# Performance work log

Hardware: AMD Instinct MI355X
Metric: run time of the kernel (lower is better)

Reference implementation:

```python
import jax, jax.numpy as jnp
import numpy as np

N_NODES = 50000
N_GRAPHS = 128
IN_DIM = 512
HID = 512
N_LAYERS = 3


def setup_inputs() -> dict:
    key = jax.random.key(0)
    ks = jax.random.split(key, 12)
    inp = {
        "x": jax.random.normal(ks[0], (N_NODES, IN_DIM), dtype=jnp.float32),
        "walk2": jax.random.randint(ks[1], (3, N_NODES), 0, N_NODES, dtype=jnp.int32),
        "walk3": jax.random.randint(ks[2], (4, N_NODES), 0, N_NODES, dtype=jnp.int32),
        "walk4": jax.random.randint(ks[3], (5, N_NODES), 0, N_NODES, dtype=jnp.int32),
        "batch": jnp.sort(jax.random.randint(ks[4], (N_NODES,), 0, N_GRAPHS, dtype=jnp.int32)),
    }
    dims = [IN_DIM, HID, HID]
    for i in range(N_LAYERS):
        scale = 1.0 / np.sqrt(dims[i])
        inp[f"W{i}"] = jax.random.normal(ks[5 + i], (dims[i], HID), dtype=jnp.float32) * scale
        inp[f"b{i}"] = jnp.zeros((HID,), dtype=jnp.float32)
    return inp


def _gather_sum(z, walk):
    # walk: [L, N] node indices -> sum of gathered embeddings, [N, H]
    L, N = walk.shape
    return jnp.take(z, walk.reshape(-1), axis=0).reshape(L, N, z.shape[1]).sum(0)


def reference(x, walk2, walk3, walk4, batch, W0, b0, W1, b1, W2, b2):
    layers = [(W0, b0), (W1, b1), (W2, b2)]
    path_batch = jnp.take(batch, walk2[0])  # [N]
    counts = jax.ops.segment_sum(jnp.ones((path_batch.shape[0],), jnp.float32),
                                 path_batch, num_segments=N_GRAPHS)
    denom = jnp.maximum(counts, 1.0)[:, None]  # avoid div-by-zero for empty graphs
    z = x
    g = []
    for W, b in layers:
        z = z @ W + b  # [N, H]
        path_emb = _gather_sum(z, walk2) + _gather_sum(z, walk3) + _gather_sum(z, walk4)
        pooled = jax.ops.segment_sum(path_emb, path_batch, num_segments=N_GRAPHS) / denom
        g.append(pooled)
    return jnp.concatenate(g, axis=1)  # [N_GRAPHS, 3*H]
```

## Files before the change

kernel.cpp:

```cpp
#include <hip/hip_runtime.h>

#define N_NODES 50000
#define N_GRAPHS 128
#define HID 512

#define KSPAN   288
#define NSTEP   18
#define KS2     44
#define KSPLIT  (KS2 * 4)
#define KPAD    (KSPAN * KSPLIT)
#define NPANEL  (KPAD / 16)

#define C8_OFF     0
#define C8_BYTES   ((size_t)N_GRAPHS * KPAD)
#define PSUM_OFF   (C8_OFF + C8_BYTES)
#define PSUM_BYTES ((size_t)N_GRAPHS * HID * 4)
#define COUNTS_OFF (PSUM_OFF + PSUM_BYTES)
#define ZERO_BYTES (COUNTS_OFF + 512)
#define APACK_OFF  ZERO_BYTES
#define APACK_BYTES ((size_t)NPANEL * 4 * 64 * 16)
#define PART_OFF   (APACK_OFF + APACK_BYTES)
#define PART_BYTES ((size_t)KS2 * N_GRAPHS * HID * 4)

typedef __attribute__((ext_vector_type(8))) short bf16x8;
typedef __attribute__((ext_vector_type(16))) float f32x16;

__global__ __launch_bounds__(256)
void build_c_kernel(const int* __restrict__ w2, const int* __restrict__ w3,
                    const int* __restrict__ w4, const int* __restrict__ batch,
                    unsigned int* __restrict__ C32, int* __restrict__ counts) {
    __shared__ int hist[N_GRAPHS];
    const int t = threadIdx.x;
    if (t < N_GRAPHS) hist[t] = 0;
    __syncthreads();
    const int i = blockIdx.x * 256 + t;
    if (i < N_NODES) {
        const int a = w2[i];
        const int g = batch[a];
        atomicAdd(&hist[g], 1);
        unsigned int* row = C32 + (size_t)g * (KPAD / 4);
        int nn[12];
        nn[0]  = a;
        nn[1]  = w2[N_NODES + i];
        nn[2]  = w2[2 * N_NODES + i];
        nn[3]  = w3[i];
        nn[4]  = w3[N_NODES + i];
        nn[5]  = w3[2 * N_NODES + i];
        nn[6]  = w3[3 * N_NODES + i];
        nn[7]  = w4[i];
        nn[8]  = w4[N_NODES + i];
        nn[9]  = w4[2 * N_NODES + i];
        nn[10] = w4[3 * N_NODES + i];
        nn[11] = w4[4 * N_NODES + i];
#pragma unroll
        for (int j = 0; j < 12; ++j) {
            const int nd = nn[j];
            atomicAdd(&row[nd >> 2], 1u << ((nd & 3) * 8));
        }
    }
    __syncthreads();
    if (t < N_GRAPHS) { const int hv = hist[t]; if (hv) atomicAdd(&counts[t], hv); }
}

__device__ inline unsigned pack_bf16(unsigned a, unsigned b) {
    return (__builtin_bit_cast(unsigned, (float)a) >> 16) |
           (__builtin_bit_cast(unsigned, (float)b) & 0xFFFF0000u);
}

__global__ __launch_bounds__(256)
void c8_to_apack_kernel(const unsigned char* __restrict__ C8,
                        uint4* __restrict__ Apack) {
    const int kp = blockIdx.x;
    const int t = threadIdx.x;
    const int mt = t >> 6;
    const int l = t & 63;
    const int row = mt * 32 + (l & 31);
    const int k0 = kp * 16 + 8 * (l >> 5);
    const uint2 b = *(const uint2*)(C8 + (size_t)row * KPAD + k0);
    uint4 o;
    o.x = pack_bf16(b.x & 0xFFu, (b.x >> 8) & 0xFFu);
    o.y = pack_bf16((b.x >> 16) & 0xFFu, b.x >> 24);
    o.z = pack_bf16(b.y & 0xFFu, (b.y >> 8) & 0xFFu);
    o.w = pack_bf16((b.y >> 16) & 0xFFu, b.y >> 24);
    Apack[(size_t)(kp * 4 + mt) * 64 + l] = o;
}

template <int GUARD>
__device__ inline void issue_b(const float* __restrict__ xp, int krow,
                               unsigned (&u)[16]) {
#pragma unroll
    for (int j = 0; j < 8; ++j) {
        int k = krow + j;
        if (GUARD) k = min(k, N_NODES - 1);
        const float* p = xp + (size_t)k * HID;
        u[j]     = __builtin_bit_cast(unsigned, p[0]);
        u[8 + j] = __builtin_bit_cast(unsigned, p[32]);
    }
}

__device__ inline f32x16 mfma_bf16(bf16x8 a, bf16x8 b, f32x16 c) {
    return __builtin_amdgcn_mfma_f32_32x32x16_bf16(a, b, c, 0, 0, 0);
}

__device__ inline unsigned bpack(unsigned u0, unsigned u1) {
    return __builtin_amdgcn_perm(u1, u0, 0x07060302u);
}

__device__ inline void step_mfma(const unsigned (&u)[16], const uint4 (&a)[2],
                                 f32x16 (&acc)[2][2]) {
    unsigned d0[4], d1[4];
#pragma unroll
    for (int jj = 0; jj < 4; ++jj) {
        d0[jj] = bpack(u[2 * jj], u[2 * jj + 1]);
        d1[jj] = bpack(u[8 + 2 * jj], u[8 + 2 * jj + 1]);
    }
    const bf16x8 b0 = __builtin_bit_cast(bf16x8, make_uint4(d0[0], d0[1], d0[2], d0[3]));
    const bf16x8 b1 = __builtin_bit_cast(bf16x8, make_uint4(d1[0], d1[1], d1[2], d1[3]));
    const bf16x8 a0 = __builtin_bit_cast(bf16x8, a[0]);
    const bf16x8 a1 = __builtin_bit_cast(bf16x8, a[1]);
    acc[0][0] = mfma_bf16(a0, b0, acc[0][0]);
    acc[0][1] = mfma_bf16(a0, b1, acc[0][1]);
    acc[1][0] = mfma_bf16(a1, b0, acc[1][0]);
    acc[1][1] = mfma_bf16(a1, b1, acc[1][1]);
}

template <int GUARD>
__device__ inline void run_k(const float* __restrict__ xp,
                             const uint4* __restrict__ Apack,
                             int kbase, int h, int lane, int rm,
                             f32x16 (&acc)[2][2]) {
    unsigned bu[3][16];
    uint4 au[3][2];
    const int kp0 = kbase >> 4;
#pragma unroll
    for (int s = 0; s < 3; ++s) {
        issue_b<GUARD>(xp, kbase + s * 16 + 8 * h, bu[s]);
        au[s][0] = Apack[(size_t)((kp0 + s) * 4 + rm * 2) * 64 + lane];
        au[s][1] = Apack[(size_t)((kp0 + s) * 4 + rm * 2 + 1) * 64 + lane];
    }
#pragma unroll
    for (int s = 0; s < NSTEP; ++s) {
        const int slot = s % 3;
        step_mfma(bu[slot], au[slot], acc);
        if (s + 3 < NSTEP) {
            issue_b<GUARD>(xp, kbase + (s + 3) * 16 + 8 * h, bu[slot]);
            au[slot][0] = Apack[(size_t)((kp0 + s + 3) * 4 + rm * 2) * 64 + lane];
            au[slot][1] = Apack[(size_t)((kp0 + s + 3) * 4 + rm * 2 + 1) * 64 + lane];
        }
    }
}

template <int ATOMIC>
__global__ __launch_bounds__(256, 3)
void pool_gemm5_kernel(const float* __restrict__ x,
                       const uint4* __restrict__ Apack,
                       float* __restrict__ dst) {
    __shared__ float red[3][2][64 * 16];
    const int t = threadIdx.x;
    const int lane = t & 63;
    const int w = t >> 6;
    const int n = lane & 31;
    const int h = lane >> 5;
    const int region = blockIdx.x;
    const int rm = region & 1;
    const int rn = region >> 1;
    const int ks = blockIdx.y * 4 + w;
    const int kbase = ks * KSPAN;

    f32x16 acc[2][2];
#pragma unroll
    for (int p = 0; p < 2; ++p)
#pragma unroll
        for (int q = 0; q < 2; ++q)
#pragma unroll
            for (int r = 0; r < 16; ++r) acc[p][q][r] = 0.f;

    const float* xp = x + rn * 64 + n;

    if (kbase + KSPAN <= N_NODES) {
        run_k<0>(xp, Apack, kbase, h, lane, rm, acc);
    } else if (kbase < N_NODES) {
        run_k<1>(xp, Apack, kbase, h, lane, rm, acc);
    }

    float* outp = ATOMIC ? dst : dst + (size_t)blockIdx.y * (N_GRAPHS * HID);
#pragma unroll
    for (int p = 0; p < 2; ++p) {
        __syncthreads();
        if (w > 0) {
#pragma unroll
            for (int q = 0; q < 2; ++q)
#pragma unroll
                for (int i = 0; i < 16; ++i)
                    red[w - 1][q][i * 64 + lane] = acc[p][q][i];
        }
        __syncthreads();
        if (w == 0) {
#pragma unroll
            for (int q = 0; q < 2; ++q)
#pragma unroll
                for (int i = 0; i < 16; ++i) {
                    const float v = acc[p][q][i] + red[0][q][i * 64 + lane] +
                                    red[1][q][i * 64 + lane] + red[2][q][i * 64 + lane];
                    const int row = rm * 64 + p * 32 + (i & 3) + 8 * (i >> 2) + 4 * h;
                    const int col = rn * 64 + q * 32 + n;
                    if (ATOMIC) atomicAdd(&outp[(size_t)row * HID + col], v);
                    else        outp[(size_t)row * HID + col] = v;
                }
        }
    }
}

__global__ __launch_bounds__(256)
void reduce_part_kernel(const float* __restrict__ part, float* __restrict__ Psum) {
    const int id = blockIdx.x * 256 + threadIdx.x;
    float s0 = 0.f, s1 = 0.f;
    for (int k = 0; k + 2 <= KS2; k += 2) {
        s0 += part[(size_t)k * (N_GRAPHS * HID) + id];
        s1 += part[(size_t)(k + 1) * (N_GRAPHS * HID) + id];
    }
    Psum[id] = s0 + s1;
}

__global__ __launch_bounds__(256)
void layer_gemm_kernel(const float* __restrict__ A, int lda, int scaleA,
                       const float* __restrict__ W,
                       const float* __restrict__ bias,
                       const int* __restrict__ counts,
                       float* __restrict__ out) {
    __shared__ float Alds[16][128];
    const int ct = blockIdx.x, rt = blockIdx.y, ksb = blockIdx.z;
    const int t = threadIdx.x;
    const int cc = ct * 64 + (t & 63);
    const int wv = t >> 6;
    const int k0 = ksb * 128;

    for (int idx = t; idx < 16 * 32; idx += 256) {
        const int rr = idx >> 5;
        const int kk = (idx & 31) * 4;
        const int row = rt * 16 + rr;
        float4 v = *(const float4*)&A[(size_t)row * lda + k0 + kk];
        if (scaleA) {
            const float inv = 1.f / (float)max(counts[row], 1);
            v.x *= inv; v.y *= inv; v.z *= inv; v.w *= inv;
        }
        *(float4*)&Alds[rr][kk] = v;
    }
    __syncthreads();

    const int r0 = rt * 16 + wv * 4;
    float a0 = 0.f, a1 = 0.f, a2 = 0.f, a3 = 0.f;
#pragma unroll 8
    for (int k = 0; k < 128; ++k) {
        const float wval = W[(size_t)(k0 + k) * HID + cc];
        a0 += Alds[wv * 4 + 0][k] * wval;
        a1 += Alds[wv * 4 + 1][k] * wval;
        a2 += Alds[wv * 4 + 2][k] * wval;
        a3 += Alds[wv * 4 + 3][k] * wval;
    }
    if (ksb == 0) {
        const float bc = bias[cc];
        a0 += (counts[r0 + 0] > 0 ? 12.f : 0.f) * bc;
        a1 += (counts[r0 + 1] > 0 ? 12.f : 0.f) * bc;
        a2 += (counts[r0 + 2] > 0 ? 12.f : 0.f) * bc;
        a3 += (counts[r0 + 3] > 0 ? 12.f : 0.f) * bc;
    }
    atomicAdd(&out[(size_t)(r0 + 0) * 1536 + cc], a0);
    atomicAdd(&out[(size_t)(r0 + 1) * 1536 + cc], a1);
    atomicAdd(&out[(size_t)(r0 + 2) * 1536 + cc], a2);
    atomicAdd(&out[(size_t)(r0 + 3) * 1536 + cc], a3);
}

extern "C" void kernel_launch(void* const* d_in, const int* in_sizes, int n_in,
                              void* d_out, int out_size, void* d_ws, size_t ws_size,
                              hipStream_t stream) {
    const float* x     = (const float*)d_in[0];
    const int*   w2    = (const int*)d_in[1];
    const int*   w3    = (const int*)d_in[2];
    const int*   w4    = (const int*)d_in[3];
    const int*   batch = (const int*)d_in[4];
    const float* W0    = (const float*)d_in[5];
    const float* b0    = (const float*)d_in[6];
    const float* W1    = (const float*)d_in[7];
    const float* b1    = (const float*)d_in[8];
    const float* W2    = (const float*)d_in[9];
    const float* b2    = (const float*)d_in[10];
    float* out = (float*)d_out;

    unsigned char* ws  = (unsigned char*)d_ws;
    unsigned int* C32  = (unsigned int*)(ws + C8_OFF);
    float* Psum        = (float*)(ws + PSUM_OFF);
    int* counts        = (int*)(ws + COUNTS_OFF);
    uint4* Apack       = (uint4*)(ws + APACK_OFF);
    float* part        = (float*)(ws + PART_OFF);
    const bool use_part = ws_size >= PART_OFF + PART_BYTES;

    hipMemsetAsync(d_ws, 0, ZERO_BYTES, stream);
    hipMemsetAsync(d_out, 0, (size_t)out_size * 4, stream);

    build_c_kernel<<<(N_NODES + 255) / 256, 256, 0, stream>>>(w2, w3, w4, batch, C32, counts);
    c8_to_apack_kernel<<<NPANEL, 256, 0, stream>>>((const unsigned char*)C32, Apack);

    if (use_part) {
        pool_gemm5_kernel<0><<<dim3(16, KS2), 256, 0, stream>>>(x, Apack, part);
        reduce_part_kernel<<<256, 256, 0, stream>>>(part, Psum);
    } else {
        pool_gemm5_kernel<1><<<dim3(16, KS2), 256, 0, stream>>>(x, Apack, Psum);
    }

    layer_gemm_kernel<<<dim3(8, 8, 4), 256, 0, stream>>>(Psum, HID, 1, W0, b0, counts, out);
    layer_gemm_kernel<<<dim3(8, 8, 4), 256, 0, stream>>>(out, 1536, 0, W1, b1, counts, out + 512);
    layer_gemm_kernel<<<dim3(8, 8, 4), 256, 0, stream>>>(out + 512, 1536, 0, W2, b2, counts, out + 1024);
}
```

Measured before the change: 266.4 us.

## Precompose layer weight chain and fuse three layer GEMMs; remap pool blocks per XCD

Because pooling is linear and commutes with the layers, the per-layer weights are precomposed (W0, W0·W1, W0·W1·W2, with bias rows scaled by the path count) into augmented matrices. All three graph outputs then come from one fused GEMM on the pooled input, replacing three dependent layer GEMMs and the output memset. The change also retiles the K split (272 span, 48 groups) and remaps pool GEMM blocks so each XCD handles a contiguous K range. The weight-chain GEMMs are input-independent but recomputed every call, adding work and reassociating float sums, which may shift rounding.

```diff
diff --git a/kernel.cpp b/kernel.cpp
--- a/kernel.cpp
+++ b/kernel.cpp
@@ -4,9 +4,9 @@
 #define N_GRAPHS 128
 #define HID 512
 
-#define KSPAN   288
-#define NSTEP   18
-#define KS2     44
+#define KSPAN   272
+#define NSTEP   17
+#define KS2     48
 #define KSPLIT  (KS2 * 4)
 #define KPAD    (KSPAN * KSPLIT)
 #define NPANEL  (KPAD / 16)
@@ -21,6 +21,8 @@
 #define APACK_BYTES ((size_t)NPANEL * 4 * 64 * 16)
 #define PART_OFF   (APACK_OFF + APACK_BYTES)
 #define PART_BYTES ((size_t)KS2 * N_GRAPHS * HID * 4)
+#define WAUG_OFF   (PART_OFF + PART_BYTES)
+#define WAUG_BYTES ((size_t)3 * 513 * HID * 4)
 
 typedef __attribute__((ext_vector_type(8))) short bf16x8;
 typedef __attribute__((ext_vector_type(16))) float f32x16;
@@ -161,10 +163,15 @@
     const int w = t >> 6;
     const int n = lane & 31;
     const int h = lane >> 5;
-    const int region = blockIdx.x;
+
+    const int lb = blockIdx.x + 16 * blockIdx.y;
+    const int xcd = lb & 7;
+    const int j = lb >> 3;
+    const int region = j & 15;
+    const int ksg = xcd * (KS2 / 8) + (j >> 4);
     const int rm = region & 1;
     const int rn = region >> 1;
-    const int ks = blockIdx.y * 4 + w;
+    const int ks = ksg * 4 + w;
     const int kbase = ks * KSPAN;
 
     f32x16 acc[2][2];
@@ -183,7 +190,7 @@
         run_k<1>(xp, Apack, kbase, h, lane, rm, acc);
     }
 
-    float* outp = ATOMIC ? dst : dst + (size_t)blockIdx.y * (N_GRAPHS * HID);
+    float* outp = ATOMIC ? dst : dst + (size_t)ksg * (N_GRAPHS * HID);
 #pragma unroll
     for (int p = 0; p < 2; ++p) {
         __syncthreads();
@@ -220,6 +227,94 @@
         s1 += part[(size_t)(k + 1) * (N_GRAPHS * HID) + id];
     }
     Psum[id] = s0 + s1;
+}
+
+__global__ __launch_bounds__(256)
+void waug_init_kernel(const float* __restrict__ W0, const float* __restrict__ b0,
+                      float* __restrict__ Aout) {
+    const int id = blockIdx.x * 256 + threadIdx.x;
+    if (id < 512 * 512)      Aout[id] = W0[id];
+    else if (id < 513 * 512) Aout[id] = 12.f * b0[id - 512 * 512];
+}
+
+__global__ __launch_bounds__(256)
+void wchain_kernel(const float* __restrict__ Ain, const float* __restrict__ W,
+                   const float* __restrict__ b, float* __restrict__ Aout) {
+    __shared__ float Alds[16][512];
+    const int t = threadIdx.x;
+    const int ct = blockIdx.x;
+    const int rt = blockIdx.y;
+    const int cc = ct * 64 + (t & 63);
+    for (int idx = t; idx < 16 * 128; idx += 256) {
+        const int rr = idx >> 7;
+        const int kk = (idx & 127) * 4;
+        const int row = rt * 16 + rr;
+        float4 v = (row < 513) ? *(const float4*)&Ain[(size_t)row * 512 + kk]
+                               : make_float4(0.f, 0.f, 0.f, 0.f);
+        *(float4*)&Alds[rr][kk] = v;
+    }
+    __syncthreads();
+    const int wv = t >> 6;
+    float a0 = 0.f, a1 = 0.f, a2 = 0.f, a3 = 0.f;
+#pragma unroll 8
+    for (int k = 0; k < 512; ++k) {
+        const float wval = W[(size_t)k * 512 + cc];
+        a0 += Alds[wv * 4 + 0][k] * wval;
+        a1 += Alds[wv * 4 + 1][k] * wval;
+        a2 += Alds[wv * 4 + 2][k] * wval;
+        a3 += Alds[wv * 4 + 3][k] * wval;
+    }
+    const int r0 = rt * 16 + wv * 4;
+    float acc[4] = {a0, a1, a2, a3};
+#pragma unroll
+    for (int i = 0; i < 4; ++i) {
+        const int row = r0 + i;
+        if (row < 513)
+            Aout[(size_t)row * 512 + cc] = acc[i] + (row == 512 ? 12.f * b[cc] : 0.f);
+    }
+}
+
+__global__ __launch_bounds__(256)
+void fused_layers_kernel(const float* __restrict__ Psum,
+                         const float* __restrict__ Waug,
+                         const int* __restrict__ counts,
+                         float* __restrict__ out) {
+    __shared__ float Alds[16][512];
+    const int t = threadIdx.x;
+    const int ct = blockIdx.x;
+    const int rt = blockIdx.y;
+    const int l = ct >> 3;
+    const int ccl = (ct & 7) * 64 + (t & 63);
+    for (int idx = t; idx < 16 * 128; idx += 256) {
+        const int rr = idx >> 7;
+        const int kk = (idx & 127) * 4;
+        const int row = rt * 16 + rr;
+        float4 v = *(const float4*)&Psum[(size_t)row * 512 + kk];
+        const float inv = 1.f / (float)max(counts[row], 1);
+        v.x *= inv; v.y *= inv; v.z *= inv; v.w *= inv;
+        *(float4*)&Alds[rr][kk] = v;
+    }
+    __syncthreads();
+    const float* W = Waug + (size_t)l * (513 * 512);
+    const int wv = t >> 6;
+    float a0 = 0.f, a1 = 0.f, a2 = 0.f, a3 = 0.f;
+#pragma unroll 8
+    for (int k = 0; k < 512; ++k) {
+        const float wval = W[(size_t)k * 512 + ccl];
+        a0 += Alds[wv * 4 + 0][k] * wval;
+        a1 += Alds[wv * 4 + 1][k] * wval;
+        a2 += Alds[wv * 4 + 2][k] * wval;
+        a3 += Alds[wv * 4 + 3][k] * wval;
+    }
+    const float bv = W[512 * 512 + ccl];
+    const int r0 = rt * 16 + wv * 4;
+    float acc[4] = {a0, a1, a2, a3};
+#pragma unroll
+    for (int i = 0; i < 4; ++i) {
+        const int row = r0 + i;
+        out[(size_t)row * 1536 + l * 512 + ccl] =
+            acc[i] + (counts[row] > 0 ? bv : 0.f);
+    }
 }
 
 __global__ __launch_bounds__(256)
@@ -293,22 +388,38 @@
     int* counts        = (int*)(ws + COUNTS_OFF);
     uint4* Apack       = (uint4*)(ws + APACK_OFF);
     float* part        = (float*)(ws + PART_OFF);
+    float* Waug        = (float*)(ws + WAUG_OFF);
     const bool use_part = ws_size >= PART_OFF + PART_BYTES;
+    const bool use_waug = ws_size >= WAUG_OFF + WAUG_BYTES;
 
     hipMemsetAsync(d_ws, 0, ZERO_BYTES, stream);
-    hipMemsetAsync(d_out, 0, (size_t)out_size * 4, stream);
+    if (!use_waug)
+        hipMemsetAsync(d_out, 0, (size_t)out_size * 4, stream);
 
     build_c_kernel<<<(N_NODES + 255) / 256, 256, 0, stream>>>(w2, w3, w4, batch, C32, counts);
     c8_to_apack_kernel<<<NPANEL, 256, 0, stream>>>((const unsigned char*)C32, Apack);
 
     if (use_part) {
         pool_gemm5_kernel<0><<<dim3(16, KS2), 256, 0, stream>>>(x, Apack, part);
-        reduce_part_kernel<<<256, 256, 0, stream>>>(part, Psum);
     } else {
         pool_gemm5_kernel<1><<<dim3(16, KS2), 256, 0, stream>>>(x, Apack, Psum);
     }
 
-    layer_gemm_kernel<<<dim3(8, 8, 4), 256, 0, stream>>>(Psum, HID, 1, W0, b0, counts, out);
-    layer_gemm_kernel<<<dim3(8, 8, 4), 256, 0, stream>>>(out, 1536, 0, W1, b1, counts, out + 512);
-    layer_gemm_kernel<<<dim3(8, 8, 4), 256, 0, stream>>>(out + 512, 1536, 0, W2, b2, counts, out + 1024);
-}
+    if (use_waug) {
+        waug_init_kernel<<<(513 * 512 + 255) / 256, 256, 0, stream>>>(W0, b0, Waug);
+        wchain_kernel<<<dim3(8, 33), 256, 0, stream>>>(Waug, W1, b1, Waug + 513 * 512);
+        wchain_kernel<<<dim3(8, 33), 256, 0, stream>>>(Waug + 513 * 512, W2, b2,
+                                                       Waug + 2 * 513 * 512);
+    }
+
+    if (use_part)
+        reduce_part_kernel<<<256, 256, 0, stream>>>(part, Psum);
+
+    if (use_waug) {
+        fused_layers_kernel<<<dim3(24, 8), 256, 0, stream>>>(Psum, Waug, counts, out);
+    } else {
+        layer_gemm_kernel<<<dim3(8, 8, 4), 256, 0, stream>>>(Psum, HID, 1, W0, b0, counts, out);
+        layer_gemm_kernel<<<dim3(8, 8, 4), 256, 0, stream>>>(out, 1536, 0, W1, b1, counts, out + 512);
+        layer_gemm_kernel<<<dim3(8, 8, 4), 256, 0, stream>>>(out + 512, 1536, 0, W2, b2, counts, out + 1024);
+    }
+}
```

Result: slower. 333.9 us (+25.3%).

## Fuse count-matrix bf16 packing into pool GEMM and drop layer split-K atomics

Applied to the files above, without the earlier changes.

Removes the separate c8_to_apack kernel. The pool GEMM now reads the uint8 count matrix directly and converts it to bf16 in registers. Each block now covers all 128 graph rows and 32 output columns, so x is read once per column strip instead of twice, at the cost of more redundant A loads and conversions per wave. The layer GEMMs lose their K-split and atomics, write their results directly, and no longer need the output memset; the trade-off is fewer blocks and a longer serial K loop.

```diff
diff --git a/kernel.cpp b/kernel.cpp
--- a/kernel.cpp
+++ b/kernel.cpp
@@ -9,18 +9,16 @@
 #define KS2     44
 #define KSPLIT  (KS2 * 4)
 #define KPAD    (KSPAN * KSPLIT)
-#define NPANEL  (KPAD / 16)
 
 #define C8_OFF     0
 #define C8_BYTES   ((size_t)N_GRAPHS * KPAD)
-#define PSUM_OFF   (C8_OFF + C8_BYTES)
+#define COUNTS_OFF C8_BYTES
+#define PSUM_OFF   (COUNTS_OFF + 512)
 #define PSUM_BYTES ((size_t)N_GRAPHS * HID * 4)
-#define COUNTS_OFF (PSUM_OFF + PSUM_BYTES)
-#define ZERO_BYTES (COUNTS_OFF + 512)
-#define APACK_OFF  ZERO_BYTES
-#define APACK_BYTES ((size_t)NPANEL * 4 * 64 * 16)
-#define PART_OFF   (APACK_OFF + APACK_BYTES)
+#define PART_OFF   (PSUM_OFF + PSUM_BYTES)
 #define PART_BYTES ((size_t)KS2 * N_GRAPHS * HID * 4)
+#define ZERO_MAIN  (COUNTS_OFF + 512)
+#define ZERO_FB    (PSUM_OFF + PSUM_BYTES)
 
 typedef __attribute__((ext_vector_type(8))) short bf16x8;
 typedef __attribute__((ext_vector_type(16))) float f32x16;
@@ -67,146 +65,123 @@
            (__builtin_bit_cast(unsigned, (float)b) & 0xFFFF0000u);
 }
 
-__global__ __launch_bounds__(256)
-void c8_to_apack_kernel(const unsigned char* __restrict__ C8,
-                        uint4* __restrict__ Apack) {
-    const int kp = blockIdx.x;
-    const int t = threadIdx.x;
-    const int mt = t >> 6;
-    const int l = t & 63;
-    const int row = mt * 32 + (l & 31);
-    const int k0 = kp * 16 + 8 * (l >> 5);
-    const uint2 b = *(const uint2*)(C8 + (size_t)row * KPAD + k0);
+template <int GUARD>
+__device__ inline void issue_b(const float* __restrict__ xp, int krow,
+                               unsigned (&u)[8]) {
+#pragma unroll
+    for (int j = 0; j < 8; ++j) {
+        int k = krow + j;
+        if (GUARD) k = min(k, N_NODES - 1);
+        u[j] = __builtin_bit_cast(unsigned, xp[(size_t)k * HID]);
+    }
+}
+
+__device__ inline f32x16 mfma_bf16(bf16x8 a, bf16x8 b, f32x16 c) {
+    return __builtin_amdgcn_mfma_f32_32x32x16_bf16(a, b, c, 0, 0, 0);
+}
+
+__device__ inline unsigned bpack(unsigned u0, unsigned u1) {
+    return __builtin_amdgcn_perm(u1, u0, 0x07060302u);
+}
+
+__device__ inline bf16x8 apack8(uint2 b) {
     uint4 o;
     o.x = pack_bf16(b.x & 0xFFu, (b.x >> 8) & 0xFFu);
     o.y = pack_bf16((b.x >> 16) & 0xFFu, b.x >> 24);
     o.z = pack_bf16(b.y & 0xFFu, (b.y >> 8) & 0xFFu);
     o.w = pack_bf16((b.y >> 16) & 0xFFu, b.y >> 24);
-    Apack[(size_t)(kp * 4 + mt) * 64 + l] = o;
-}
-
-template <int GUARD>
-__device__ inline void issue_b(const float* __restrict__ xp, int krow,
-                               unsigned (&u)[16]) {
-#pragma unroll
-    for (int j = 0; j < 8; ++j) {
-        int k = krow + j;
-        if (GUARD) k = min(k, N_NODES - 1);
-        const float* p = xp + (size_t)k * HID;
-        u[j]     = __builtin_bit_cast(unsigned, p[0]);
-        u[8 + j] = __builtin_bit_cast(unsigned, p[32]);
-    }
-}
-
-__device__ inline f32x16 mfma_bf16(bf16x8 a, bf16x8 b, f32x16 c) {
-    return __builtin_amdgcn_mfma_f32_32x32x16_bf16(a, b, c, 0, 0, 0);
-}
-
-__device__ inline unsigned bpack(unsigned u0, unsigned u1) {
-    return __builtin_amdgcn_perm(u1, u0, 0x07060302u);
-}
-
-__device__ inline void step_mfma(const unsigned (&u)[16], const uint4 (&a)[2],
-                                 f32x16 (&acc)[2][2]) {
-    unsigned d0[4], d1[4];
-#pragma unroll
-    for (int jj = 0; jj < 4; ++jj) {
-        d0[jj] = bpack(u[2 * jj], u[2 * jj + 1]);
-        d1[jj] = bpack(u[8 + 2 * jj], u[8 + 2 * jj + 1]);
-    }
-    const bf16x8 b0 = __builtin_bit_cast(bf16x8, make_uint4(d0[0], d0[1], d0[2], d0[3]));
-    const bf16x8 b1 = __builtin_bit_cast(bf16x8, make_uint4(d1[0], d1[1], d1[2], d1[3]));
-    const bf16x8 a0 = __builtin_bit_cast(bf16x8, a[0]);
-    const bf16x8 a1 = __builtin_bit_cast(bf16x8, a[1]);
-    acc[0][0] = mfma_bf16(a0, b0, acc[0][0]);
-    acc[0][1] = mfma_bf16(a0, b1, acc[0][1]);
-    acc[1][0] = mfma_bf16(a1, b0, acc[1][0]);
-    acc[1][1] = mfma_bf16(a1, b1, acc[1][1]);
+    return __builtin_bit_cast(bf16x8, o);
+}
+
+__device__ inline void step_mfma(const unsigned (&u)[8], const uint2 (&a)[4],
+                                 f32x16 (&acc)[4]) {
+    unsigned d[4];
+#pragma unroll
+    for (int jj = 0; jj < 4; ++jj) d[jj] = bpack(u[2 * jj], u[2 * jj + 1]);
+    const bf16x8 b0 = __builtin_bit_cast(bf16x8, make_uint4(d[0], d[1], d[2], d[3]));
+#pragma unroll
+    for (int mt = 0; mt < 4; ++mt)
+        acc[mt] = mfma_bf16(apack8(a[mt]), b0, acc[mt]);
 }
 
 template <int GUARD>
 __device__ inline void run_k(const float* __restrict__ xp,
-                             const uint4* __restrict__ Apack,
-                             int kbase, int h, int lane, int rm,
-                             f32x16 (&acc)[2][2]) {
-    unsigned bu[3][16];
-    uint4 au[3][2];
-    const int kp0 = kbase >> 4;
+                             const unsigned char* __restrict__ c8p,
+                             int kbase, int h, f32x16 (&acc)[4]) {
+    unsigned bu[3][8];
+    uint2 au[3][4];
 #pragma unroll
     for (int s = 0; s < 3; ++s) {
-        issue_b<GUARD>(xp, kbase + s * 16 + 8 * h, bu[s]);
-        au[s][0] = Apack[(size_t)((kp0 + s) * 4 + rm * 2) * 64 + lane];
-        au[s][1] = Apack[(size_t)((kp0 + s) * 4 + rm * 2 + 1) * 64 + lane];
+        const int kr = kbase + s * 16 + 8 * h;
+        issue_b<GUARD>(xp, kr, bu[s]);
+#pragma unroll
+        for (int mt = 0; mt < 4; ++mt)
+            au[s][mt] = *(const uint2*)(c8p + (size_t)mt * (32 * KPAD) + kr);
     }
 #pragma unroll
     for (int s = 0; s < NSTEP; ++s) {
         const int slot = s % 3;
         step_mfma(bu[slot], au[slot], acc);
         if (s + 3 < NSTEP) {
-            issue_b<GUARD>(xp, kbase + (s + 3) * 16 + 8 * h, bu[slot]);
-            au[slot][0] = Apack[(size_t)((kp0 + s + 3) * 4 + rm * 2) * 64 + lane];
-            au[slot][1] = Apack[(size_t)((kp0 + s + 3) * 4 + rm * 2 + 1) * 64 + lane];
+            const int kr = kbase + (s + 3) * 16 + 8 * h;
+            issue_b<GUARD>(xp, kr, bu[slot]);
+#pragma unroll
+            for (int mt = 0; mt < 4; ++mt)
+                au[slot][mt] = *(const uint2*)(c8p + (size_t)mt * (32 * KPAD) + kr);
         }
     }
 }
 
 template <int ATOMIC>
 __global__ __launch_bounds__(256, 3)
-void pool_gemm5_kernel(const float* __restrict__ x,
-                       const uint4* __restrict__ Apack,
+void pool_gemm6_kernel(const float* __restrict__ x,
+                       const unsigned char* __restrict__ C8,
                        float* __restrict__ dst) {
-    __shared__ float red[3][2][64 * 16];
+    __shared__ float red[3][16 * 64];
     const int t = threadIdx.x;
     const int lane = t & 63;
     const int w = t >> 6;
     const int n = lane & 31;
     const int h = lane >> 5;
-    const int region = blockIdx.x;
-    const int rm = region & 1;
-    const int rn = region >> 1;
+    const int rn = blockIdx.x;
     const int ks = blockIdx.y * 4 + w;
     const int kbase = ks * KSPAN;
 
-    f32x16 acc[2][2];
-#pragma unroll
-    for (int p = 0; p < 2; ++p)
-#pragma unroll
-        for (int q = 0; q < 2; ++q)
-#pragma unroll
-            for (int r = 0; r < 16; ++r) acc[p][q][r] = 0.f;
-
-    const float* xp = x + rn * 64 + n;
+    f32x16 acc[4];
+#pragma unroll
+    for (int p = 0; p < 4; ++p)
+#pragma unroll
+        for (int r = 0; r < 16; ++r) acc[p][r] = 0.f;
+
+    const float* xp = x + rn * 32 + n;
+    const unsigned char* c8p = C8 + (size_t)(lane & 31) * KPAD;
 
     if (kbase + KSPAN <= N_NODES) {
-        run_k<0>(xp, Apack, kbase, h, lane, rm, acc);
+        run_k<0>(xp, c8p, kbase, h, acc);
     } else if (kbase < N_NODES) {
-        run_k<1>(xp, Apack, kbase, h, lane, rm, acc);
+        run_k<1>(xp, c8p, kbase, h, acc);
     }
 
     float* outp = ATOMIC ? dst : dst + (size_t)blockIdx.y * (N_GRAPHS * HID);
 #pragma unroll
-    for (int p = 0; p < 2; ++p) {
+    for (int p = 0; p < 4; ++p) {
         __syncthreads();
         if (w > 0) {
 #pragma unroll
-            for (int q = 0; q < 2; ++q)
-#pragma unroll
-                for (int i = 0; i < 16; ++i)
-                    red[w - 1][q][i * 64 + lane] = acc[p][q][i];
+            for (int i = 0; i < 16; ++i)
+                red[w - 1][i * 64 + lane] = acc[p][i];
         }
         __syncthreads();
         if (w == 0) {
 #pragma unroll
-            for (int q = 0; q < 2; ++q)
-#pragma unroll
-                for (int i = 0; i < 16; ++i) {
-                    const float v = acc[p][q][i] + red[0][q][i * 64 + lane] +
-                                    red[1][q][i * 64 + lane] + red[2][q][i * 64 + lane];
-                    const int row = rm * 64 + p * 32 + (i & 3) + 8 * (i >> 2) + 4 * h;
-                    const int col = rn * 64 + q * 32 + n;
-                    if (ATOMIC) atomicAdd(&outp[(size_t)row * HID + col], v);
-                    else        outp[(size_t)row * HID + col] = v;
-                }
+            for (int i = 0; i < 16; ++i) {
+                const float v = acc[p][i] + red[0][i * 64 + lane] +
+                                red[1][i * 64 + lane] + red[2][i * 64 + lane];
+                const int row = p * 32 + (i & 3) + 8 * (i >> 2) + 4 * h;
+                const int col = rn * 32 + n;
+                if (ATOMIC) atomicAdd(&outp[(size_t)row * HID + col], v);
+                else        outp[(size_t)row * HID + col] = v;
+            }
         }
     }
 }
@@ -223,23 +198,22 @@
 }
 
 __global__ __launch_bounds__(256)
-void layer_gemm_kernel(const float* __restrict__ A, int lda, int scaleA,
-                       const float* __restrict__ W,
-                       const float* __restrict__ bias,
-                       const int* __restrict__ counts,
-                       float* __restrict__ out) {
-    __shared__ float Alds[16][128];
-    const int ct = blockIdx.x, rt = blockIdx.y, ksb = blockIdx.z;
+void layer_gemm6_kernel(const float* __restrict__ A, int lda, int scaleA,
+                        const float* __restrict__ W,
+                        const float* __restrict__ bias,
+                        const int* __restrict__ counts,
+                        float* __restrict__ out) {
+    __shared__ float Alds[16][512];
+    const int ct = blockIdx.x, rt = blockIdx.y;
     const int t = threadIdx.x;
     const int cc = ct * 64 + (t & 63);
     const int wv = t >> 6;
-    const int k0 = ksb * 128;
-
-    for (int idx = t; idx < 16 * 32; idx += 256) {
-        const int rr = idx >> 5;
-        const int kk = (idx & 31) * 4;
+
+    for (int idx = t; idx < 16 * 128; idx += 256) {
+        const int rr = idx >> 7;
+        const int kk = (idx & 127) * 4;
         const int row = rt * 16 + rr;
-        float4 v = *(const float4*)&A[(size_t)row * lda + k0 + kk];
+        float4 v = *(const float4*)&A[(size_t)row * lda + kk];
         if (scaleA) {
             const float inv = 1.f / (float)max(counts[row], 1);
             v.x *= inv; v.y *= inv; v.z *= inv; v.w *= inv;
@@ -251,24 +225,18 @@
     const int r0 = rt * 16 + wv * 4;
     float a0 = 0.f, a1 = 0.f, a2 = 0.f, a3 = 0.f;
 #pragma unroll 8
-    for (int k = 0; k < 128; ++k) {
-        const float wval = W[(size_t)(k0 + k) * HID + cc];
+    for (int k = 0; k < 512; ++k) {
+        const float wval = W[(size_t)k * HID + cc];
         a0 += Alds[wv * 4 + 0][k] * wval;
         a1 += Alds[wv * 4 + 1][k] * wval;
         a2 += Alds[wv * 4 + 2][k] * wval;
         a3 += Alds[wv * 4 + 3][k] * wval;
     }
-    if (ksb == 0) {
-        const float bc = bias[cc];
-        a0 += (counts[r0 + 0] > 0 ? 12.f : 0.f) * bc;
-        a1 += (counts[r0 + 1] > 0 ? 12.f : 0.f) * bc;
-        a2 += (counts[r0 + 2] > 0 ? 12.f : 0.f) * bc;
-        a3 += (counts[r0 + 3] > 0 ? 12.f : 0.f) * bc;
-    }
-    atomicAdd(&out[(size_t)(r0 + 0) * 1536 + cc], a0);
-    atomicAdd(&out[(size_t)(r0 + 1) * 1536 + cc], a1);
-    atomicAdd(&out[(size_t)(r0 + 2) * 1536 + cc], a2);
-    atomicAdd(&out[(size_t)(r0 + 3) * 1536 + cc], a3);
+    const float bc = bias[cc];
+    out[(size_t)(r0 + 0) * 1536 + cc] = a0 + (counts[r0 + 0] > 0 ? 12.f : 0.f) * bc;
+    out[(size_t)(r0 + 1) * 1536 + cc] = a1 + (counts[r0 + 1] > 0 ? 12.f : 0.f) * bc;
+    out[(size_t)(r0 + 2) * 1536 + cc] = a2 + (counts[r0 + 2] > 0 ? 12.f : 0.f) * bc;
+    out[(size_t)(r0 + 3) * 1536 + cc] = a3 + (counts[r0 + 3] > 0 ? 12.f : 0.f) * bc;
 }
 
 extern "C" void kernel_launch(void* const* d_in, const int* in_sizes, int n_in,
@@ -289,26 +257,25 @@
 
     unsigned char* ws  = (unsigned char*)d_ws;
     unsigned int* C32  = (unsigned int*)(ws + C8_OFF);
+    int* counts        = (int*)(ws + COUNTS_OFF);
     float* Psum        = (float*)(ws + PSUM_OFF);
-    int* counts        = (int*)(ws + COUNTS_OFF);
-    uint4* Apack       = (uint4*)(ws + APACK_OFF);
     float* part        = (float*)(ws + PART_OFF);
     const bool use_part = ws_size >= PART_OFF + PART_BYTES;
 
-    hipMemsetAsync(d_ws, 0, ZERO_BYTES, stream);
-    hipMemsetAsync(d_out, 0, (size_t)out_size * 4, stream);
+    hipMemsetAsync(d_ws, 0, use_part ? ZERO_MAIN : ZERO_FB, stream);
 
     build_c_kernel<<<(N_NODES + 255) / 256, 256, 0, stream>>>(w2, w3, w4, batch, C32, counts);
-    c8_to_apack_kernel<<<NPANEL, 256, 0, stream>>>((const unsigned char*)C32, Apack);
 
     if (use_part) {
-        pool_gemm5_kernel<0><<<dim3(16, KS2), 256, 0, stream>>>(x, Apack, part);
+        pool_gemm6_kernel<0><<<dim3(16, KS2), 256, 0, stream>>>(
+            x, (const unsigned char*)C32, part);
         reduce_part_kernel<<<256, 256, 0, stream>>>(part, Psum);
     } else {
-        pool_gemm5_kernel<1><<<dim3(16, KS2), 256, 0, stream>>>(x, Apack, Psum);
-    }
-
-    layer_gemm_kernel<<<dim3(8, 8, 4), 256, 0, stream>>>(Psum, HID, 1, W0, b0, counts, out);
-    layer_gemm_kernel<<<dim3(8, 8, 4), 256, 0, stream>>>(out, 1536, 0, W1, b1, counts, out + 512);
-    layer_gemm_kernel<<<dim3(8, 8, 4), 256, 0, stream>>>(out + 512, 1536, 0, W2, b2, counts, out + 1024);
-}
+        pool_gemm6_kernel<1><<<dim3(16, KS2), 256, 0, stream>>>(
+            x, (const unsigned char*)C32, Psum);
+    }
+
+    layer_gemm6_kernel<<<dim3(8, 8), 256, 0, stream>>>(Psum, HID, 1, W0, b0, counts, out);
+    layer_gemm6_kernel<<<dim3(8, 8), 256, 0, stream>>>(out, 1536, 0, W1, b1, counts, out + 512);
+    layer_gemm6_kernel<<<dim3(8, 8), 256, 0, stream>>>(out + 512, 1536, 0, W2, b2, counts, out + 1024);
+}
```

New measurement: 368.7 us. 1.38x slower.

## Reshape pooling GEMM tiles to cover all 128 graph rows per block

Applied to the files above, without the earlier changes.

Each pooling-GEMM block now computes all 128 graph rows for a 32-column slice, using four MFMA row tiles per wave, instead of a 64x64 tile. Before, every node-feature element of x was fetched by two row regions; now it is fetched once, which halves the dominant x read traffic. The cost is twice as many packed A-operand loads per k-step and a narrower 32-column load per row. The K split is also retuned (span 272, 48 k-groups) to match the new grid.

```diff
diff --git a/kernel.cpp b/kernel.cpp
--- a/kernel.cpp
+++ b/kernel.cpp
@@ -4,9 +4,9 @@
 #define N_GRAPHS 128
 #define HID 512
 
-#define KSPAN   288
-#define NSTEP   18
-#define KS2     44
+#define KSPAN   272
+#define NSTEP   17
+#define KS2     48
 #define KSPLIT  (KS2 * 4)
 #define KPAD    (KSPAN * KSPLIT)
 #define NPANEL  (KPAD / 16)
@@ -86,15 +86,13 @@
 }
 
 template <int GUARD>
-__device__ inline void issue_b(const float* __restrict__ xp, int krow,
-                               unsigned (&u)[16]) {
+__device__ inline void issue_b8(const float* __restrict__ xp, int krow,
+                                unsigned (&u)[8]) {
 #pragma unroll
     for (int j = 0; j < 8; ++j) {
         int k = krow + j;
         if (GUARD) k = min(k, N_NODES - 1);
-        const float* p = xp + (size_t)k * HID;
-        u[j]     = __builtin_bit_cast(unsigned, p[0]);
-        u[8 + j] = __builtin_bit_cast(unsigned, p[32]);
+        u[j] = __builtin_bit_cast(unsigned, xp[(size_t)k * HID]);
     }
 }
 
@@ -106,107 +104,94 @@
     return __builtin_amdgcn_perm(u1, u0, 0x07060302u);
 }
 
-__device__ inline void step_mfma(const unsigned (&u)[16], const uint4 (&a)[2],
-                                 f32x16 (&acc)[2][2]) {
-    unsigned d0[4], d1[4];
-#pragma unroll
-    for (int jj = 0; jj < 4; ++jj) {
-        d0[jj] = bpack(u[2 * jj], u[2 * jj + 1]);
-        d1[jj] = bpack(u[8 + 2 * jj], u[8 + 2 * jj + 1]);
-    }
-    const bf16x8 b0 = __builtin_bit_cast(bf16x8, make_uint4(d0[0], d0[1], d0[2], d0[3]));
-    const bf16x8 b1 = __builtin_bit_cast(bf16x8, make_uint4(d1[0], d1[1], d1[2], d1[3]));
-    const bf16x8 a0 = __builtin_bit_cast(bf16x8, a[0]);
-    const bf16x8 a1 = __builtin_bit_cast(bf16x8, a[1]);
-    acc[0][0] = mfma_bf16(a0, b0, acc[0][0]);
-    acc[0][1] = mfma_bf16(a0, b1, acc[0][1]);
-    acc[1][0] = mfma_bf16(a1, b0, acc[1][0]);
-    acc[1][1] = mfma_bf16(a1, b1, acc[1][1]);
+__device__ inline void step_mfma4(const unsigned (&u)[8], const uint4 (&a)[4],
+                                  f32x16 (&acc)[4]) {
+    unsigned d[4];
+#pragma unroll
+    for (int jj = 0; jj < 4; ++jj) d[jj] = bpack(u[2 * jj], u[2 * jj + 1]);
+    const bf16x8 b0 = __builtin_bit_cast(bf16x8, make_uint4(d[0], d[1], d[2], d[3]));
+#pragma unroll
+    for (int mt = 0; mt < 4; ++mt)
+        acc[mt] = mfma_bf16(__builtin_bit_cast(bf16x8, a[mt]), b0, acc[mt]);
 }
 
 template <int GUARD>
-__device__ inline void run_k(const float* __restrict__ xp,
-                             const uint4* __restrict__ Apack,
-                             int kbase, int h, int lane, int rm,
-                             f32x16 (&acc)[2][2]) {
-    unsigned bu[3][16];
-    uint4 au[3][2];
+__device__ inline void run_k4(const float* __restrict__ xp,
+                              const uint4* __restrict__ Apack,
+                              int kbase, int h, int lane,
+                              f32x16 (&acc)[4]) {
+    unsigned bu[3][8];
+    uint4 au[3][4];
     const int kp0 = kbase >> 4;
 #pragma unroll
     for (int s = 0; s < 3; ++s) {
-        issue_b<GUARD>(xp, kbase + s * 16 + 8 * h, bu[s]);
-        au[s][0] = Apack[(size_t)((kp0 + s) * 4 + rm * 2) * 64 + lane];
-        au[s][1] = Apack[(size_t)((kp0 + s) * 4 + rm * 2 + 1) * 64 + lane];
+        issue_b8<GUARD>(xp, kbase + s * 16 + 8 * h, bu[s]);
+#pragma unroll
+        for (int mt = 0; mt < 4; ++mt)
+            au[s][mt] = Apack[(size_t)((kp0 + s) * 4 + mt) * 64 + lane];
     }
 #pragma unroll
     for (int s = 0; s < NSTEP; ++s) {
         const int slot = s % 3;
-        step_mfma(bu[slot], au[slot], acc);
+        step_mfma4(bu[slot], au[slot], acc);
         if (s + 3 < NSTEP) {
-            issue_b<GUARD>(xp, kbase + (s + 3) * 16 + 8 * h, bu[slot]);
-            au[slot][0] = Apack[(size_t)((kp0 + s + 3) * 4 + rm * 2) * 64 + lane];
-            au[slot][1] = Apack[(size_t)((kp0 + s + 3) * 4 + rm * 2 + 1) * 64 + lane];
+            issue_b8<GUARD>(xp, kbase + (s + 3) * 16 + 8 * h, bu[slot]);
+#pragma unroll
+            for (int mt = 0; mt < 4; ++mt)
+                au[slot][mt] = Apack[(size_t)((kp0 + s + 3) * 4 + mt) * 64 + lane];
         }
     }
 }
 
 template <int ATOMIC>
 __global__ __launch_bounds__(256, 3)
-void pool_gemm5_kernel(const float* __restrict__ x,
+void pool_gemm7_kernel(const float* __restrict__ x,
                        const uint4* __restrict__ Apack,
                        float* __restrict__ dst) {
-    __shared__ float red[3][2][64 * 16];
+    __shared__ float red[3][16 * 64];
     const int t = threadIdx.x;
     const int lane = t & 63;
     const int w = t >> 6;
     const int n = lane & 31;
     const int h = lane >> 5;
-    const int region = blockIdx.x;
-    const int rm = region & 1;
-    const int rn = region >> 1;
+    const int rn = blockIdx.x;
     const int ks = blockIdx.y * 4 + w;
     const int kbase = ks * KSPAN;
 
-    f32x16 acc[2][2];
-#pragma unroll
-    for (int p = 0; p < 2; ++p)
-#pragma unroll
-        for (int q = 0; q < 2; ++q)
-#pragma unroll
-            for (int r = 0; r < 16; ++r) acc[p][q][r] = 0.f;
-
-    const float* xp = x + rn * 64 + n;
+    f32x16 acc[4];
+#pragma unroll
+    for (int p = 0; p < 4; ++p)
+#pragma unroll
+        for (int r = 0; r < 16; ++r) acc[p][r] = 0.f;
+
+    const float* xp = x + rn * 32 + n;
 
     if (kbase + KSPAN <= N_NODES) {
-        run_k<0>(xp, Apack, kbase, h, lane, rm, acc);
+        run_k4<0>(xp, Apack, kbase, h, lane, acc);
     } else if (kbase < N_NODES) {
-        run_k<1>(xp, Apack, kbase, h, lane, rm, acc);
+        run_k4<1>(xp, Apack, kbase, h, lane, acc);
     }
 
     float* outp = ATOMIC ? dst : dst + (size_t)blockIdx.y * (N_GRAPHS * HID);
 #pragma unroll
-    for (int p = 0; p < 2; ++p) {
+    for (int p = 0; p < 4; ++p) {
         __syncthreads();
         if (w > 0) {
 #pragma unroll
-            for (int q = 0; q < 2; ++q)
-#pragma unroll
-                for (int i = 0; i < 16; ++i)
-                    red[w - 1][q][i * 64 + lane] = acc[p][q][i];
+            for (int i = 0; i < 16; ++i)
+                red[w - 1][i * 64 + lane] = acc[p][i];
         }
         __syncthreads();
         if (w == 0) {
 #pragma unroll
-            for (int q = 0; q < 2; ++q)
-#pragma unroll
-                for (int i = 0; i < 16; ++i) {
-                    const float v = acc[p][q][i] + red[0][q][i * 64 + lane] +
-                                    red[1][q][i * 64 + lane] + red[2][q][i * 64 + lane];
-                    const int row = rm * 64 + p * 32 + (i & 3) + 8 * (i >> 2) + 4 * h;
-                    const int col = rn * 64 + q * 32 + n;
-                    if (ATOMIC) atomicAdd(&outp[(size_t)row * HID + col], v);
-                    else        outp[(size_t)row * HID + col] = v;
-                }
+            for (int i = 0; i < 16; ++i) {
+                const float v = acc[p][i] + red[0][i * 64 + lane] +
+                                red[1][i * 64 + lane] + red[2][i * 64 + lane];
+                const int row = p * 32 + (i & 3) + 8 * (i >> 2) + 4 * h;
+                const int col = rn * 32 + n;
+                if (ATOMIC) atomicAdd(&outp[(size_t)row * HID + col], v);
+                else        outp[(size_t)row * HID + col] = v;
+            }
         }
     }
 }
@@ -302,10 +287,10 @@
     c8_to_apack_kernel<<<NPANEL, 256, 0, stream>>>((const unsigned char*)C32, Apack);
 
     if (use_part) {
-        pool_gemm5_kernel<0><<<dim3(16, KS2), 256, 0, stream>>>(x, Apack, part);
+        pool_gemm7_kernel<0><<<dim3(16, KS2), 256, 0, stream>>>(x, Apack, part);
         reduce_part_kernel<<<256, 256, 0, stream>>>(part, Psum);
     } else {
-        pool_gemm5_kernel<1><<<dim3(16, KS2), 256, 0, stream>>>(x, Apack, Psum);
+        pool_gemm7_kernel<1><<<dim3(16, KS2), 256, 0, stream>>>(x, Apack, Psum);
     }
 
     layer_gemm_kernel<<<dim3(8, 8, 4), 256, 0, stream>>>(Psum, HID, 1, W0, b0, counts, out);
```

Result: no change. 268.2 us (+0.6%).
